# Optimization experiments

Measured on AMD Instinct MI355X. Metric: run time of the kernel, lower is better.

The kernel has to match this reference:

```python
import jax, jax.numpy as jnp
import numpy as np

SCALE = 0.02  # init scale for weight matrices


def setup_inputs() -> dict:
    B, M, H = 2048, 64, 1024
    key = jax.random.key(0)
    ks = jax.random.split(key, 10)
    inp = {
        "pose_embed": jax.random.normal(ks[0], (B, H), jnp.float32),
        "query_embed": jax.random.normal(ks[1], (B, H), jnp.float32),
        "h": jax.random.normal(ks[2], (B, H), jnp.float32),
        "c": jax.random.normal(ks[3], (B, H), jnp.float32),
        "memory": jax.random.normal(ks[4], (B, M, H), jnp.float32),
        "W_ih": jax.random.normal(ks[5], (4 * H, H), jnp.float32) * SCALE,
        "W_hh": jax.random.normal(ks[6], (4 * H, H), jnp.float32) * SCALE,
        "b_ih": jnp.zeros((4 * H,), jnp.float32),
        "b_hh": jnp.zeros((4 * H,), jnp.float32),
        "Wq": jax.random.normal(ks[7], (H, H), jnp.float32) * SCALE,
        "bq": jnp.zeros((H,), jnp.float32),
        "Wk": jax.random.normal(ks[8], (H, H), jnp.float32) * SCALE,
        "bk": jnp.zeros((H,), jnp.float32),
        "Wv": jax.random.normal(ks[9], (H, H), jnp.float32) * SCALE,
        "bv": jnp.zeros((H,), jnp.float32),
    }
    return inp


def reference(pose_embed, query_embed, h, c, memory,
              W_ih, W_hh, b_ih, b_hh, Wq, bq, Wk, bk, Wv, bv):
    H = pose_embed.shape[-1]
    # --- LSTMCell step (torch gate order: i, f, g, o) ---
    gates = pose_embed @ W_ih.T + b_ih + h @ W_hh.T + b_hh  # [B, 4H]
    i_g, f_g, g_g, o_g = jnp.split(gates, 4, axis=-1)
    c_new = jax.nn.sigmoid(f_g) * c + jax.nn.sigmoid(i_g) * jnp.tanh(g_g)
    h_new = jax.nn.sigmoid(o_g) * jnp.tanh(c_new)
    # --- FIFO memory update (detach, pop oldest, append new h) ---
    mem = jnp.concatenate(
        [memory[:, 1:], jax.lax.stop_gradient(h_new)[:, None]], axis=1)  # [B, M, H]
    # --- single-query attention over memory ---
    Q = query_embed @ Wq.T + bq                       # [B, H]
    K = mem @ Wk.T + bk                               # [B, M, H]
    V = mem @ Wv.T + bv                               # [B, M, H]
    scores = jnp.einsum('bh,bmh->bm', Q, K) / jnp.sqrt(jnp.float32(H))
    attn = jax.nn.softmax(scores, axis=-1)            # [B, M]
    attended = jnp.einsum('bm,bmh->bh', attn, V)      # [B, H]
    return attended, h_new, c_new
```

## Files before the change

### kernel.cpp

```cpp
#include <hip/hip_runtime.h>
#include <stdint.h>

typedef __attribute__((ext_vector_type(8))) short short8;
typedef __attribute__((ext_vector_type(4))) float f32x4;
typedef unsigned short u16;

__device__ __forceinline__ u16 f2bf(float f) {
  union { float f; uint32_t u; } v; v.f = f;
  return (u16)((v.u + 0x7FFFu + ((v.u >> 16) & 1u)) >> 16);
}
__device__ __forceinline__ float bf2f(u16 u) {
  union { uint32_t u; float f; } v; v.u = (uint32_t)u << 16; return v.f;
}

__device__ __forceinline__ void gl_lds16(const void* g, void* l) {
  __builtin_amdgcn_global_load_lds(
      (const __attribute__((address_space(1))) void*)g,
      (__attribute__((address_space(3))) void*)l, 16, 0, 0);
}

__global__ __launch_bounds__(256) void gemm_bt(
    const u16* __restrict__ A, const u16* __restrict__ B,
    float* __restrict__ Cf, u16* __restrict__ Cb,
    const float* __restrict__ bias1,
    int M, int N, int K)
{
  __shared__ __align__(16) u16 As[128 * 32];
  __shared__ __align__(16) u16 Bs[128 * 32];
  const int t = threadIdx.x;
  const int lane = t & 63;
  const int w = t >> 6;
  const int wr = w >> 1, wc = w & 1;
  const int m0 = blockIdx.y * 128, n0 = blockIdx.x * 128;
  const int lr = lane & 15;
  const int lk = (lane >> 4) * 8;
  const int srow = t >> 2;
  const int scol = (t & 3) * 8;

  const u16* gA = A + (size_t)(m0 + srow) * K + scol;
  const u16* gB = B + (size_t)(n0 + srow) * K + scol;

  f32x4 acc[4][4] = {};

  for (int k0 = 0; k0 < K; k0 += 32) {
    gl_lds16(gA,                  As + t * 8);
    gl_lds16(gA + (size_t)64 * K, As + 2048 + t * 8);
    gl_lds16(gB,                  Bs + t * 8);
    gl_lds16(gB + (size_t)64 * K, Bs + 2048 + t * 8);
    gA += 32; gB += 32;
    __syncthreads();

    short8 a[4], b[4];
#pragma unroll
    for (int m = 0; m < 4; ++m)
      a[m] = *(const short8*)(As + (wr * 64 + m * 16 + lr) * 32 + lk);
#pragma unroll
    for (int n = 0; n < 4; ++n)
      b[n] = *(const short8*)(Bs + (wc * 64 + n * 16 + lr) * 32 + lk);
#pragma unroll
    for (int m = 0; m < 4; ++m)
#pragma unroll
      for (int n = 0; n < 4; ++n)
        acc[m][n] = __builtin_amdgcn_mfma_f32_16x16x32_bf16(a[m], b[n], acc[m][n], 0, 0, 0);
    __syncthreads();
  }

#pragma unroll
  for (int n = 0; n < 4; ++n) {
    int col = n0 + wc * 64 + n * 16 + lr;
    float bsum = bias1 ? bias1[col] : 0.f;
#pragma unroll
    for (int m = 0; m < 4; ++m) {
#pragma unroll
      for (int r = 0; r < 4; ++r) {
        int row = m0 + wr * 64 + m * 16 + (lane >> 4) * 4 + r;
        float vv = acc[m][n][r] + bsum;
        if (Cf) Cf[(size_t)row * N + col] = vv;
        if (Cb) Cb[(size_t)row * N + col] = f2bf(vv);
      }
    }
  }
}

__global__ __launch_bounds__(512) void gates_k(
    const u16* __restrict__ Xcat, const u16* __restrict__ Wcat,
    u16* __restrict__ gparts)
{
  __shared__ __align__(16) u16 As[256 * 32];
  __shared__ __align__(16) u16 Bs[256 * 32];
  const int t = threadIdx.x;
  const int lane = t & 63;
  const int w = t >> 6;
  const int wr = w >> 2, wc = w & 3;
  const int bid = blockIdx.x;
  const int swz = (bid & 7) * 32 + (bid >> 3);
  const int m0 = (swz >> 5) * 256;
  const int rest = swz & 31;
  const int n0 = (rest >> 1) * 256;
  const int khalf = rest & 1;
  const int lr = lane & 15;
  const int lk = (lane >> 4) * 8;
  const int srow = t >> 2;
  const int scol = (t & 3) * 8;

  const u16* gA = Xcat + (size_t)(m0 + srow) * 2048 + khalf * 1024 + scol;
  const u16* gB = Wcat + (size_t)(n0 + srow) * 2048 + khalf * 1024 + scol;

  f32x4 acc[8][4] = {};
  for (int k0 = 0; k0 < 1024; k0 += 32) {
    gl_lds16(gA,                       As + t * 8);
    gl_lds16(gA + (size_t)128 * 2048,  As + 4096 + t * 8);
    gl_lds16(gB,                       Bs + t * 8);
    gl_lds16(gB + (size_t)128 * 2048,  Bs + 4096 + t * 8);
    gA += 32; gB += 32;
    __syncthreads();
    short8 b[4];
#pragma unroll
    for (int n = 0; n < 4; ++n)
      b[n] = *(const short8*)(Bs + (wc * 64 + n * 16 + lr) * 32 + lk);
#pragma unroll
    for (int m = 0; m < 8; ++m) {
      short8 a = *(const short8*)(As + (wr * 128 + m * 16 + lr) * 32 + lk);
#pragma unroll
      for (int n = 0; n < 4; ++n)
        acc[m][n] = __builtin_amdgcn_mfma_f32_16x16x32_bf16(a, b[n], acc[m][n], 0, 0, 0);
    }
    __syncthreads();
  }
  u16* out = gparts + (size_t)khalf * 2048 * 4096;
#pragma unroll
  for (int n = 0; n < 4; ++n) {
    int col = n0 + wc * 64 + n * 16 + lr;
#pragma unroll
    for (int m = 0; m < 8; ++m)
#pragma unroll
      for (int r = 0; r < 4; ++r) {
        int row = m0 + wr * 128 + m * 16 + (lane >> 4) * 4 + r;
        out[(size_t)row * 4096 + col] = f2bf(acc[m][n][r]);
      }
  }
}

__global__ __launch_bounds__(256) void attn_k(
    const float* __restrict__ Qk, const float* __restrict__ mem,
    float* __restrict__ attst)
{
  const int t = threadIdx.x;
  const int lane = t & 63;
  const int b = blockIdx.x * 4 + (t >> 6);
  const float* q = Qk + (size_t)b * 1024;
  f32x4 qv[4];
#pragma unroll
  for (int i = 0; i < 4; ++i)
    qv[i] = *(const f32x4*)(q + (i * 64 + lane) * 4);
  const float* mb = mem + (size_t)b * 65536;

  float m_run = -3e38f, l = 0.f;
  f32x4 cx[4] = {};

  for (int qd = 0; qd < 15; ++qd) {
    const float* r0 = mb + (size_t)(1 + qd * 4) * 1024;
    f32x4 rv[4][4];
    float s[4] = {0.f, 0.f, 0.f, 0.f};
#pragma unroll
    for (int rr = 0; rr < 4; ++rr)
#pragma unroll
      for (int i = 0; i < 4; ++i) {
        rv[rr][i] = __builtin_nontemporal_load(
            (const f32x4*)(r0 + rr * 1024 + (i * 64 + lane) * 4));
        s[rr] += rv[rr][i][0] * qv[i][0] + rv[rr][i][1] * qv[i][1] +
                 rv[rr][i][2] * qv[i][2] + rv[rr][i][3] * qv[i][3];
      }
#pragma unroll
    for (int rr = 0; rr < 4; ++rr) {
#pragma unroll
      for (int off = 32; off; off >>= 1) s[rr] += __shfl_xor(s[rr], off);
      s[rr] *= 0.03125f;
    }
#pragma unroll
    for (int rr = 0; rr < 4; ++rr) {
      if (s[rr] <= m_run + 8.f) {
        float e = __expf(s[rr] - m_run);
        l += e;
#pragma unroll
        for (int i = 0; i < 4; ++i) cx[i] += rv[rr][i] * e;
      } else {
        float sc = __expf(m_run - s[rr]);
        m_run = s[rr];
        l = l * sc + 1.f;
#pragma unroll
        for (int i = 0; i < 4; ++i) cx[i] = cx[i] * sc + rv[rr][i];
      }
    }
  }
  for (int r = 61; r <= 63; ++r) {
    const float* row = mb + (size_t)r * 1024;
    f32x4 rv[4];
    float s = 0.f;
#pragma unroll
    for (int i = 0; i < 4; ++i) {
      rv[i] = __builtin_nontemporal_load(
          (const f32x4*)(row + (i * 64 + lane) * 4));
      s += rv[i][0] * qv[i][0] + rv[i][1] * qv[i][1] +
           rv[i][2] * qv[i][2] + rv[i][3] * qv[i][3];
    }
#pragma unroll
    for (int off = 32; off; off >>= 1) s += __shfl_xor(s, off);
    s *= 0.03125f;
    if (s <= m_run + 8.f) {
      float e = __expf(s - m_run);
      l += e;
#pragma unroll
      for (int i = 0; i < 4; ++i) cx[i] += rv[i] * e;
    } else {
      float sc = __expf(m_run - s);
      m_run = s;
      l = l * sc + 1.f;
#pragma unroll
      for (int i = 0; i < 4; ++i) cx[i] = cx[i] * sc + rv[i];
    }
  }
  float* st = attst + (size_t)b * 1032;
#pragma unroll
  for (int i = 0; i < 4; ++i)
    *(f32x4*)(st + (i * 64 + lane) * 4) = cx[i];
  if (lane == 0) { st[1024] = m_run; st[1025] = l; }
}

__global__ __launch_bounds__(256) void prep_k(
    const float* __restrict__ pose, const float* __restrict__ h,
    const float* __restrict__ W_ih, const float* __restrict__ W_hh,
    const float* __restrict__ query, const float* __restrict__ Wv,
    const float* __restrict__ Wq, const float* __restrict__ Wk,
    u16* __restrict__ xcat, u16* __restrict__ wcat,
    u16* __restrict__ qry, u16* __restrict__ wvb,
    u16* __restrict__ wqtb, u16* __restrict__ wktb)
{
  __shared__ u16 tile[64][65];
  int blk = blockIdx.x;
  int t = threadIdx.x;
  if (blk >= 15360) {
    const float* src; u16* dst; int tblk;
    if (blk < 15616) { src = Wq; dst = wqtb; tblk = blk - 15360; }
    else             { src = Wk; dst = wktb; tblk = blk - 15616; }
    int tr = (tblk >> 4) * 64, tc = (tblk & 15) * 64;
    int tx = t & 63;
    int ty = (t >> 6) * 16;
#pragma unroll
    for (int i = 0; i < 16; ++i)
      tile[ty + i][tx] = f2bf(src[(size_t)(tr + ty + i) * 1024 + tc + tx]);
    __syncthreads();
#pragma unroll
    for (int i = 0; i < 16; ++i)
      dst[(size_t)(tc + ty + i) * 1024 + tr + tx] = tile[tx][ty + i];
    return;
  }
  const float* src; u16* dst; int ostride, ooff, base;
  if (blk < 2048)       { src = pose;  dst = xcat; ostride = 2048; ooff = 0;    base = 0; }
  else if (blk < 4096)  { src = h;     dst = xcat; ostride = 2048; ooff = 1024; base = 2048; }
  else if (blk < 8192)  { src = W_ih;  dst = wcat; ostride = 2048; ooff = 0;    base = 4096; }
  else if (blk < 12288) { src = W_hh;  dst = wcat; ostride = 2048; ooff = 1024; base = 8192; }
  else if (blk < 14336) { src = query; dst = qry;  ostride = 1024; ooff = 0;    base = 12288; }
  else                  { src = Wv;    dst = wvb;  ostride = 1024; ooff = 0;    base = 14336; }
  int r = blk - base;
  int cc = t * 4;
  float4 v = *(const float4*)(src + (size_t)r * 1024 + cc);
  ushort4 o; o.x = f2bf(v.x); o.y = f2bf(v.y); o.z = f2bf(v.z); o.w = f2bf(v.w);
  *(ushort4*)(dst + (size_t)r * ostride + ooff + cc) = o;
}

__global__ __launch_bounds__(256) void bqwk_k(
    const float* __restrict__ bq, const float* __restrict__ Wk,
    float* __restrict__ qkb)
{
  int n = blockIdx.x * 256 + threadIdx.x;
  int j0 = blockIdx.y * 64;
  float s = 0.f;
#pragma unroll 8
  for (int j = j0; j < j0 + 64; ++j) s += bq[j] * Wk[(size_t)j * 1024 + n];
  atomicAdd(&qkb[n], s);
}

__global__ __launch_bounds__(256) void lstmfin_k(
    const u16* __restrict__ gparts, const float* __restrict__ c,
    const float* __restrict__ b_ih, const float* __restrict__ b_hh,
    const float* __restrict__ Qk, const float* __restrict__ attst,
    float* __restrict__ out_h, float* __restrict__ out_c,
    u16* __restrict__ ctxb)
{
  const int b = blockIdx.x;
  const int t = threadIdx.x;
  const int lane = t & 63, wv_id = t >> 6;
  const int p = t * 4;
  const u16* g0 = gparts + (size_t)b * 4096;
  const u16* g1 = g0 + (size_t)2048 * 4096;
  float4 cv = *(const float4*)(c + (size_t)b * 1024 + p);
  float cvs[4] = {cv.x, cv.y, cv.z, cv.w};

  float hn[4], cn[4];
  float gsum[4][4];
#pragma unroll
  for (int gi = 0; gi < 4; ++gi) {
    ushort4 a = *(const ushort4*)(g0 + gi * 1024 + p);
    ushort4 bb = *(const ushort4*)(g1 + gi * 1024 + p);
    float4 bi = *(const float4*)(b_ih + gi * 1024 + p);
    float4 bh = *(const float4*)(b_hh + gi * 1024 + p);
    gsum[gi][0] = bf2f(a.x) + bf2f(bb.x) + bi.x + bh.x;
    gsum[gi][1] = bf2f(a.y) + bf2f(bb.y) + bi.y + bh.y;
    gsum[gi][2] = bf2f(a.z) + bf2f(bb.z) + bi.z + bh.z;
    gsum[gi][3] = bf2f(a.w) + bf2f(bb.w) + bi.w + bh.w;
  }
#pragma unroll
  for (int j = 0; j < 4; ++j) {
    float si = 1.f / (1.f + __expf(-gsum[0][j]));
    float sf = 1.f / (1.f + __expf(-gsum[1][j]));
    float so = 1.f / (1.f + __expf(-gsum[3][j]));
    float tg = 2.f / (1.f + __expf(-2.f * gsum[2][j])) - 1.f;
    cn[j] = sf * cvs[j] + si * tg;
    float tc2 = 2.f / (1.f + __expf(-2.f * cn[j])) - 1.f;
    hn[j] = so * tc2;
  }
  *(float4*)(out_c + (size_t)b * 1024 + p) = make_float4(cn[0], cn[1], cn[2], cn[3]);
  *(float4*)(out_h + (size_t)b * 1024 + p) = make_float4(hn[0], hn[1], hn[2], hn[3]);

  float4 qv = *(const float4*)(Qk + (size_t)b * 1024 + p);
  float part = qv.x * hn[0] + qv.y * hn[1] + qv.z * hn[2] + qv.w * hn[3];
#pragma unroll
  for (int off = 32; off; off >>= 1) part += __shfl_xor(part, off);
  __shared__ float red[4];
  if (lane == 0) red[wv_id] = part;
  __syncthreads();
  float s_last = (red[0] + red[1] + red[2] + red[3]) * 0.03125f;

  const float* st = attst + (size_t)b * 1032;
  float m_run = st[1024], l = st[1025];
  float4 cx = *(const float4*)(st + p);
  if (s_last <= m_run + 8.f) {
    float e = __expf(s_last - m_run);
    l += e;
    cx.x += e * hn[0]; cx.y += e * hn[1]; cx.z += e * hn[2]; cx.w += e * hn[3];
  } else {
    float sc = __expf(m_run - s_last);
    l = l * sc + 1.f;
    cx.x = cx.x * sc + hn[0]; cx.y = cx.y * sc + hn[1];
    cx.z = cx.z * sc + hn[2]; cx.w = cx.w * sc + hn[3];
  }
  float inv = 1.f / l;
  ushort4 o;
  o.x = f2bf(cx.x * inv); o.y = f2bf(cx.y * inv);
  o.z = f2bf(cx.z * inv); o.w = f2bf(cx.w * inv);
  *(ushort4*)(ctxb + (size_t)b * 1024 + p) = o;
}

extern "C" void kernel_launch(void* const* d_in, const int* in_sizes, int n_in,
                              void* d_out, int out_size, void* d_ws, size_t ws_size,
                              hipStream_t stream) {
  const int Bb = 2048, Hh = 1024;
  const float* pose  = (const float*)d_in[0];
  const float* query = (const float*)d_in[1];
  const float* h     = (const float*)d_in[2];
  const float* c     = (const float*)d_in[3];
  const float* mem   = (const float*)d_in[4];
  const float* W_ih  = (const float*)d_in[5];
  const float* W_hh  = (const float*)d_in[6];
  const float* b_ih  = (const float*)d_in[7];
  const float* b_hh  = (const float*)d_in[8];
  const float* Wq    = (const float*)d_in[9];
  const float* bq    = (const float*)d_in[10];
  const float* Wk    = (const float*)d_in[11];
  const float* Wv    = (const float*)d_in[13];
  const float* bv    = (const float*)d_in[14];

  float* out_att = (float*)d_out;
  float* out_h   = out_att + (size_t)Bb * Hh;
  float* out_c   = out_h + (size_t)Bb * Hh;

  char* wp = (char*)d_ws;
  auto alloc = [&](size_t bytes) {
    char* p = wp; wp += (bytes + 255) & ~(size_t)255; return p;
  };
  u16*   Xcat  = (u16*)alloc((size_t)2048 * 2048 * 2);
  u16*   Wcat  = (u16*)alloc((size_t)4096 * 2048 * 2);
  u16*   Qryb  = (u16*)alloc((size_t)2048 * 1024 * 2);
  u16*   WqTb  = (u16*)alloc((size_t)1024 * 1024 * 2);
  u16*   WkTb  = (u16*)alloc((size_t)1024 * 1024 * 2);
  u16*   Gb    = (u16*)alloc((size_t)1024 * 1024 * 2);
  u16*   Wvb   = (u16*)alloc((size_t)1024 * 1024 * 2);
  u16*   gparts= (u16*)alloc((size_t)2 * 2048 * 4096 * 2);
  float* qkb   = (float*)alloc((size_t)1024 * 4);
  float* Qk    = (float*)alloc((size_t)2048 * 1024 * 4);
  u16*   ctxb  = (u16*)alloc((size_t)2048 * 1024 * 2);
  float* attst = (float*)Qryb;

  prep_k<<<15872, 256, 0, stream>>>(pose, h, W_ih, W_hh, query, Wv, Wq, Wk,
                                    Xcat, Wcat, Qryb, Wvb, WqTb, WkTb);

  hipMemsetAsync(qkb, 0, 1024 * sizeof(float), stream);
  bqwk_k<<<dim3(4, 16), 256, 0, stream>>>(bq, Wk, qkb);

  gemm_bt<<<dim3(8, 8), 256, 0, stream>>>(
      WkTb, WqTb, nullptr, Gb, nullptr, 1024, 1024, 1024);

  gemm_bt<<<dim3(8, 16), 256, 0, stream>>>(
      Qryb, Gb, Qk, nullptr, qkb, 2048, 1024, 1024);

  gates_k<<<256, 512, 0, stream>>>(Xcat, Wcat, gparts);

  attn_k<<<512, 256, 0, stream>>>(Qk, mem, attst);

  lstmfin_k<<<2048, 256, 0, stream>>>(gparts, c, b_ih, b_hh, Qk, attst,
                                      out_h, out_c, ctxb);

  gemm_bt<<<dim3(8, 16), 256, 0, stream>>>(
      ctxb, Wvb, out_att, nullptr, bv, 2048, 1024, 1024);
}
```

Measured before the change: 260.2 us.

## Double-buffer gates GEMM with 64-wide K tiles, swizzled LDS and interleaved MFMA

Rewrites the LSTM gates GEMM kernel to use two 64KB LDS buffers with 64-wide K steps. The next tile's global-to-LDS loads are issued while the current tile is computed, with explicit vmcnt waits and raw s_barriers replacing the two __syncthreads per step. The LDS layout is XOR-swizzled to avoid bank conflicts. Fragment loads are split into groups interleaved with MFMA blocks, with s_setprio raising priority around the MFMA bursts. This aims to hide memory latency, at the cost of 128KB of LDS per block, which limits occupancy to one block per CU, and it drops the old XCD-aware block remapping.

```diff
diff --git a/kernel.cpp b/kernel.cpp
--- a/kernel.cpp
+++ b/kernel.cpp
@@ -4,6 +4,10 @@
 typedef __attribute__((ext_vector_type(8))) short short8;
 typedef __attribute__((ext_vector_type(4))) float f32x4;
 typedef unsigned short u16;
+
+#define SBAR() do { __builtin_amdgcn_sched_barrier(0); \
+                    __builtin_amdgcn_s_barrier(); \
+                    __builtin_amdgcn_sched_barrier(0); } while (0)
 
 __device__ __forceinline__ u16 f2bf(float f) {
   union { float f; uint32_t u; } v; v.f = f;
@@ -82,61 +86,127 @@
   }
 }
 
-__global__ __launch_bounds__(512) void gates_k(
+__global__ __launch_bounds__(512) void gates8_k(
     const u16* __restrict__ Xcat, const u16* __restrict__ Wcat,
     u16* __restrict__ gparts)
 {
-  __shared__ __align__(16) u16 As[256 * 32];
-  __shared__ __align__(16) u16 Bs[256 * 32];
+  __shared__ __align__(16) u16 lds[65536];
   const int t = threadIdx.x;
-  const int lane = t & 63;
+  const int l = t & 63;
   const int w = t >> 6;
   const int wr = w >> 2, wc = w & 3;
   const int bid = blockIdx.x;
-  const int swz = (bid & 7) * 32 + (bid >> 3);
-  const int m0 = (swz >> 5) * 256;
-  const int rest = swz & 31;
-  const int n0 = (rest >> 1) * 256;
-  const int khalf = rest & 1;
-  const int lr = lane & 15;
-  const int lk = (lane >> 4) * 8;
-  const int srow = t >> 2;
-  const int scol = (t & 3) * 8;
-
-  const u16* gA = Xcat + (size_t)(m0 + srow) * 2048 + khalf * 1024 + scol;
-  const u16* gB = Wcat + (size_t)(n0 + srow) * 2048 + khalf * 1024 + scol;
+  const int tile = bid >> 1, khalf = bid & 1;
+  const int m0 = (tile >> 4) * 256;
+  const int n0 = (tile & 15) * 256;
+  const int lr = l & 15;
+  const int l4 = l >> 4;
+
+  const int sr = l >> 3;
+  const int sc = ((l & 7) * 8) ^ ((l >> 5) << 4);
+
+  const u16* Abase = Xcat + (size_t)m0 * 2048 + khalf * 1024 + sc;
+  const u16* Bbase = Wcat + (size_t)n0 * 2048 + khalf * 1024 + sc;
+
+  #define STAGE(buf, kt) do {                                                  \
+    const int kof_ = (kt) * 64;                                                \
+    _Pragma("unroll")                                                          \
+    for (int hh = 0; hh < 2; ++hh)                                             \
+      _Pragma("unroll")                                                        \
+      for (int j = 0; j < 2; ++j) {                                            \
+        int row_ = hh * 128 + (w + 8 * j) * 8 + sr;                            \
+        char* dA = (char*)lds + (buf) * 65536 + hh * 16384 + (w + 8*j) * 1024 + l * 16; \
+        char* dB = dA + 32768;                                                 \
+        gl_lds16(Abase + (size_t)row_ * 2048 + kof_, dA);                      \
+        gl_lds16(Bbase + (size_t)row_ * 2048 + kof_, dB);                      \
+      }                                                                        \
+  } while (0)
+
+  auto LDA = [&](int buf, int mf, int s) -> short8 {
+    int rr = mf * 16 + lr;
+    int cb = (s * 64 + l4 * 16) ^ (((rr >> 2) & 1) << 5);
+    return *(const short8*)((const char*)lds + buf * 65536 + wr * 16384 + rr * 128 + cb);
+  };
+  auto LDB = [&](int buf, int nf, int s) -> short8 {
+    int rr = (wc & 1) * 64 + nf * 16 + lr;
+    int cb = (s * 64 + l4 * 16) ^ (((rr >> 2) & 1) << 5);
+    return *(const short8*)((const char*)lds + buf * 65536 + 32768 + (wc >> 1) * 16384 + rr * 128 + cb);
+  };
 
   f32x4 acc[8][4] = {};
-  for (int k0 = 0; k0 < 1024; k0 += 32) {
-    gl_lds16(gA,                       As + t * 8);
-    gl_lds16(gA + (size_t)128 * 2048,  As + 4096 + t * 8);
-    gl_lds16(gB,                       Bs + t * 8);
-    gl_lds16(gB + (size_t)128 * 2048,  Bs + 4096 + t * 8);
-    gA += 32; gB += 32;
-    __syncthreads();
-    short8 b[4];
-#pragma unroll
-    for (int n = 0; n < 4; ++n)
-      b[n] = *(const short8*)(Bs + (wc * 64 + n * 16 + lr) * 32 + lk);
-#pragma unroll
-    for (int m = 0; m < 8; ++m) {
-      short8 a = *(const short8*)(As + (wr * 128 + m * 16 + lr) * 32 + lk);
-#pragma unroll
-      for (int n = 0; n < 4; ++n)
-        acc[m][n] = __builtin_amdgcn_mfma_f32_16x16x32_bf16(a, b[n], acc[m][n], 0, 0, 0);
-    }
-    __syncthreads();
-  }
+
+  STAGE(0, 0);
+  STAGE(1, 1);
+  asm volatile("s_waitcnt vmcnt(8)" ::: "memory");
+  SBAR();
+
+  for (int kt = 0; kt < 16; ++kt) {
+    const int cur = kt & 1;
+    short8 a0[4][2], a1[4][2], b[2][2];
+#pragma unroll
+    for (int i = 0; i < 4; ++i) { a0[i][0] = LDA(cur, i, 0); a0[i][1] = LDA(cur, i, 1); }
+#pragma unroll
+    for (int n = 0; n < 2; ++n) { b[n][0] = LDB(cur, n, 0); b[n][1] = LDB(cur, n, 1); }
+    __builtin_amdgcn_s_setprio(1);
+#pragma unroll
+    for (int i = 0; i < 4; ++i)
+#pragma unroll
+      for (int n = 0; n < 2; ++n)
+#pragma unroll
+        for (int s = 0; s < 2; ++s)
+          acc[i][n] = __builtin_amdgcn_mfma_f32_16x16x32_bf16(a0[i][s], b[n][s], acc[i][n], 0, 0, 0);
+    __builtin_amdgcn_s_setprio(0);
+#pragma unroll
+    for (int i = 0; i < 4; ++i) { a1[i][0] = LDA(cur, 4 + i, 0); a1[i][1] = LDA(cur, 4 + i, 1); }
+    __builtin_amdgcn_s_setprio(1);
+#pragma unroll
+    for (int i = 0; i < 4; ++i)
+#pragma unroll
+      for (int n = 0; n < 2; ++n)
+#pragma unroll
+        for (int s = 0; s < 2; ++s)
+          acc[4 + i][n] = __builtin_amdgcn_mfma_f32_16x16x32_bf16(a1[i][s], b[n][s], acc[4 + i][n], 0, 0, 0);
+    __builtin_amdgcn_s_setprio(0);
+#pragma unroll
+    for (int n = 0; n < 2; ++n) { b[n][0] = LDB(cur, 2 + n, 0); b[n][1] = LDB(cur, 2 + n, 1); }
+    __builtin_amdgcn_s_setprio(1);
+#pragma unroll
+    for (int i = 0; i < 4; ++i)
+#pragma unroll
+      for (int n = 0; n < 2; ++n)
+#pragma unroll
+        for (int s = 0; s < 2; ++s)
+          acc[4 + i][2 + n] = __builtin_amdgcn_mfma_f32_16x16x32_bf16(a1[i][s], b[n][s], acc[4 + i][2 + n], 0, 0, 0);
+#pragma unroll
+    for (int i = 0; i < 4; ++i)
+#pragma unroll
+      for (int n = 0; n < 2; ++n)
+#pragma unroll
+        for (int s = 0; s < 2; ++s)
+          acc[i][2 + n] = __builtin_amdgcn_mfma_f32_16x16x32_bf16(a0[i][s], b[n][s], acc[i][2 + n], 0, 0, 0);
+    __builtin_amdgcn_s_setprio(0);
+
+    SBAR();
+    if (kt + 2 < 16) {
+      STAGE(cur, kt + 2);
+      asm volatile("s_waitcnt vmcnt(8)" ::: "memory");
+    } else {
+      asm volatile("s_waitcnt vmcnt(0)" ::: "memory");
+    }
+    SBAR();
+  }
+  #undef STAGE
+
   u16* out = gparts + (size_t)khalf * 2048 * 4096;
 #pragma unroll
-  for (int n = 0; n < 4; ++n) {
-    int col = n0 + wc * 64 + n * 16 + lr;
-#pragma unroll
-    for (int m = 0; m < 8; ++m)
+  for (int nf = 0; nf < 4; ++nf) {
+    int col = n0 + wc * 64 + nf * 16 + lr;
+#pragma unroll
+    for (int mf = 0; mf < 8; ++mf)
 #pragma unroll
       for (int r = 0; r < 4; ++r) {
-        int row = m0 + wr * 128 + m * 16 + (lane >> 4) * 4 + r;
-        out[(size_t)row * 4096 + col] = f2bf(acc[m][n][r]);
+        int row = m0 + wr * 128 + mf * 16 + l4 * 4 + r;
+        out[(size_t)row * 4096 + col] = f2bf(acc[mf][nf][r]);
       }
   }
 }
@@ -404,7 +474,7 @@
   gemm_bt<<<dim3(8, 16), 256, 0, stream>>>(
       Qryb, Gb, Qk, nullptr, qkb, 2048, 1024, 1024);
 
-  gates_k<<<256, 512, 0, stream>>>(Xcat, Wcat, gparts);
+  gates8_k<<<256, 512, 0, stream>>>(Xcat, Wcat, gparts);
 
   attn_k<<<512, 256, 0, stream>>>(Qk, mem, attst);
 
```

After: 248.4 us. -4.5%, faster.
